# Kernel optimization log

Hardware: AMD Instinct MI355X
Metric: run time of the kernel (lower is better)

Reference implementation:

```python
import jax, jax.numpy as jnp
import numpy as np

B, S = 32, 512
N_CAT, P, K, D = 50000, 8, 256, 64  # n_categories, pattern_length, n_symbols, symbol_dim


def setup_inputs() -> dict:
    key = jax.random.key(0)
    k1, k2, k3 = jax.random.split(key, 3)
    inputs = jax.random.randint(k1, (B, S), 0, N_CAT)
    pattern_map = jax.random.normal(k2, (N_CAT, P, K), dtype=jnp.float32)
    symbols = jax.random.normal(k3, (K, D), dtype=jnp.float32)
    tau = jnp.ones((1,), dtype=jnp.float32)
    return {"inputs": inputs, "pattern_map": pattern_map, "symbols": symbols, "tau": tau}


def reference(inputs, pattern_map, symbols, tau):
    # Gather per-category symbol logits: [B, S, P, K]
    energies = pattern_map[inputs]
    # Gumbel-softmax with straight-through hard sampling (fixed noise key)
    g = jax.random.gumbel(jax.random.key(42), energies.shape, dtype=energies.dtype)
    soft = jax.nn.softmax((energies + g) / tau, axis=-1)
    hard = jax.nn.one_hot(jnp.argmax(soft, axis=-1), soft.shape[-1], dtype=soft.dtype)
    weights = jax.lax.stop_gradient(hard - soft) + soft  # straight-through
    # Weighted lookup of symbols: [B, S, P, D]
    embeds = jnp.einsum('bspk,kd->bspd', weights, symbols)
    # mode == 'concat': [B, S, P*D]
    b, s = inputs.shape
    return embeds.reshape(b, s, -1)
```

## Files before the change

kernel.cpp:

```cpp
#include <hip/hip_runtime.h>
#include <stdint.h>

#define NGROUPS (32 * 512 * 8)
#define WAVES_PER_BLOCK 4

#define ROTL(x, r) (((x) << (r)) | ((x) >> (32 - (r))))

__device__ __forceinline__ unsigned tf42_bits(unsigned n) {
    const unsigned K0 = 0u;
    const unsigned K1 = 42u;
    const unsigned K2 = 0x1BD11BDAu ^ 0u ^ 42u;
    unsigned x0 = 0u + K0;
    unsigned x1 = n + K1;

#define TF_ROUND(r) x0 += x1; x1 = ROTL(x1, r); x1 ^= x0;
    TF_ROUND(13) TF_ROUND(15) TF_ROUND(26) TF_ROUND(6)
    x0 += K1; x1 += K2 + 1u;
    TF_ROUND(17) TF_ROUND(29) TF_ROUND(16) TF_ROUND(24)
    x0 += K2; x1 += K0 + 2u;
    TF_ROUND(13) TF_ROUND(15) TF_ROUND(26) TF_ROUND(6)
    x0 += K0; x1 += K1 + 3u;
    TF_ROUND(17) TF_ROUND(29) TF_ROUND(16) TF_ROUND(24)
    x0 += K1; x1 += K2 + 4u;
    TF_ROUND(13) TF_ROUND(15) TF_ROUND(26) TF_ROUND(6)
    x0 += K2; x1 += K0 + 5u;
#undef TF_ROUND
    return x0 ^ x1;
}

__device__ __forceinline__ float gumbel_from_bits(unsigned bits) {
    float f = __uint_as_float((bits >> 9) | 0x3f800000u) - 1.0f;
    float u = (f == 0.0f) ? 1.17549435e-38f : f;
    return -__ocml_log_f32(-__ocml_log_f32(u));
}

extern "C" __device__ float __ocml_log_f32(float);

__global__ __launch_bounds__(256) void se_gumbel_kernel(
    const int* __restrict__ inputs,
    const float* __restrict__ pmap,
    const float* __restrict__ symbols,
    const float* __restrict__ tau,
    float* __restrict__ out)
{
    const int lane = threadIdx.x & 63;
    const int wave = threadIdx.x >> 6;
    const int group = blockIdx.x * WAVES_PER_BLOCK + wave;
    const int p  = group & 7;
    const int bs = group >> 3;

    const int cat = inputs[bs];
    const float tv = tau[0];

    const float4 e4 = *reinterpret_cast<const float4*>(
        pmap + (size_t)cat * 2048 + (size_t)p * 256 + (size_t)lane * 4);
    const float ev[4] = {e4.x, e4.y, e4.z, e4.w};

    const unsigned nbase = ((unsigned)group << 8) + (unsigned)(lane * 4);

    float best = -__builtin_inff();
    int bestk = 0;
    #pragma unroll
    for (int j = 0; j < 4; ++j) {
        const unsigned bits = tf42_bits(nbase + j);
        float f = __uint_as_float((bits >> 9) | 0x3f800000u) - 1.0f;
        float u = (f == 0.0f) ? 1.17549435e-38f : f;
        float g = -logf(-logf(u));
        float x = (ev[j] + g) / tv;
        if (x > best) { best = x; bestk = lane * 4 + j; }
    }

    #pragma unroll
    for (int off = 32; off > 0; off >>= 1) {
        float ov = __shfl_down(best, off, 64);
        int   ok = __shfl_down(bestk, off, 64);
        if (ov > best || (ov == best && ok < bestk)) { best = ov; bestk = ok; }
    }
    bestk = __shfl(bestk, 0, 64);

    out[(size_t)group * 64 + lane] = symbols[(size_t)bestk * 64 + lane];
}

extern "C" void kernel_launch(void* const* d_in, const int* in_sizes, int n_in,
                              void* d_out, int out_size, void* d_ws, size_t ws_size,
                              hipStream_t stream) {
    const int*   inputs  = (const int*)d_in[0];
    const float* pmap    = (const float*)d_in[1];
    const float* symbols = (const float*)d_in[2];
    const float* tau     = (const float*)d_in[3];
    float* out = (float*)d_out;

    const int n_blocks = NGROUPS / WAVES_PER_BLOCK;
    hipLaunchKernelGGL(se_gumbel_kernel, dim3(n_blocks), dim3(256), 0, stream,
                       inputs, pmap, symbols, tau, out);
}
```

Baseline: 521.8 us.

## Use fast log2 Gumbel approximation with precise refinement near the max

Computes the Gumbel noise with hardware log2 intrinsics, falling back to precise logf only when u is near 1. A wave max reduction sets a threshold band, and only candidates within the band are recomputed precisely for the argmax. Division by tau is replaced with a sign factor, since argmax only depends on tau's sign. This cuts transcendental cost but adds an extra reduction pass and relies on the band being wide enough to keep the argmax exact.

After: 514.0 us. About the same (-1.5%).

```diff
diff --git a/kernel.cpp b/kernel.cpp
--- a/kernel.cpp
+++ b/kernel.cpp
@@ -12,7 +12,6 @@
     const unsigned K2 = 0x1BD11BDAu ^ 0u ^ 42u;
     unsigned x0 = 0u + K0;
     unsigned x1 = n + K1;
-
 #define TF_ROUND(r) x0 += x1; x1 = ROTL(x1, r); x1 ^= x0;
     TF_ROUND(13) TF_ROUND(15) TF_ROUND(26) TF_ROUND(6)
     x0 += K1; x1 += K2 + 1u;
@@ -28,13 +27,19 @@
     return x0 ^ x1;
 }
 
-__device__ __forceinline__ float gumbel_from_bits(unsigned bits) {
+__device__ __forceinline__ float u_from_bits(unsigned bits) {
     float f = __uint_as_float((bits >> 9) | 0x3f800000u) - 1.0f;
-    float u = (f == 0.0f) ? 1.17549435e-38f : f;
-    return -__ocml_log_f32(-__ocml_log_f32(u));
+    return (f == 0.0f) ? 1.17549435e-38f : f;
 }
 
-extern "C" __device__ float __ocml_log_f32(float);
+__device__ __forceinline__ float precise_g(unsigned bits) {
+    float u = u_from_bits(bits);
+    return -logf(-logf(u));
+}
+
+#define NLN2 (-0.693147180559945f)
+#define BAND 0.015625f
+#define L2U_NEAR1 (-1.220703125e-4f)
 
 __global__ __launch_bounds__(256) void se_gumbel_kernel(
     const int* __restrict__ inputs,
@@ -50,7 +55,7 @@
     const int bs = group >> 3;
 
     const int cat = inputs[bs];
-    const float tv = tau[0];
+    const float rs = (tau[0] > 0.0f) ? 1.0f : -1.0f;
 
     const float4 e4 = *reinterpret_cast<const float4*>(
         pmap + (size_t)cat * 2048 + (size_t)p * 256 + (size_t)lane * 4);
@@ -58,16 +63,40 @@
 
     const unsigned nbase = ((unsigned)group << 8) + (unsigned)(lane * 4);
 
-    float best = -__builtin_inff();
-    int bestk = 0;
+    unsigned bits[4];
+    float xt[4];
+    float lmax = -__builtin_inff();
     #pragma unroll
     for (int j = 0; j < 4; ++j) {
-        const unsigned bits = tf42_bits(nbase + j);
-        float f = __uint_as_float((bits >> 9) | 0x3f800000u) - 1.0f;
-        float u = (f == 0.0f) ? 1.17549435e-38f : f;
-        float g = -logf(-logf(u));
-        float x = (ev[j] + g) / tv;
-        if (x > best) { best = x; bestk = lane * 4 + j; }
+        bits[j] = tf42_bits(nbase + j);
+        float u = u_from_bits(bits[j]);
+        float l2u = __builtin_amdgcn_logf(u);
+        float x;
+        if (l2u > L2U_NEAR1) {
+            x = rs * (ev[j] + precise_g(bits[j]));
+        } else {
+            float L = l2u * NLN2;
+            float g = __builtin_amdgcn_logf(L) * NLN2;
+            x = rs * (ev[j] + g);
+        }
+        xt[j] = x;
+        lmax = fmaxf(lmax, x);
+    }
+
+    #pragma unroll
+    for (int off = 32; off > 0; off >>= 1)
+        lmax = fmaxf(lmax, __shfl_down(lmax, off, 64));
+    const float T = __shfl(lmax, 0, 64) - BAND;
+
+    float best = -__builtin_inff();
+    int bestk = 0x7fffffff;
+    #pragma unroll
+    for (int j = 0; j < 4; ++j) {
+        if (xt[j] >= T) {
+            float px = rs * (ev[j] + precise_g(bits[j]));
+            int k = lane * 4 + j;
+            if (px > best || (px == best && k < bestk)) { best = px; bestk = k; }
+        }
     }
 
     #pragma unroll
```
